# Kernel tuning notes

Hardware: AMD Instinct MI355X
Metric: run time of the kernel (lower is better)

The kernel has to match this reference:

```python
import jax, jax.numpy as jnp
import numpy as np

B, T, CIN = 32, 16384, 32
COUT, NB, NA = 32, 3, 2


def setup_inputs() -> dict:
    key = jax.random.key(0)
    k1, k2, k3, k4 = jax.random.split(key, 4)
    u = jax.random.normal(k1, (B, T, CIN), dtype=jnp.float32)
    x0 = jax.random.normal(k2, (B, NA, COUT), dtype=jnp.float32)
    # AR coeffs scaled small so the length-16384 IIR recurrence is stable
    a_coeff = jax.random.normal(k3, (NA, COUT), dtype=jnp.float32) * 0.05
    b_coeff = jax.random.normal(k4, (NB, CIN, COUT), dtype=jnp.float32)
    return {"u": u, "x0": x0, "a_coeff": a_coeff, "b_coeff": b_coeff}


def reference(u, x0, a_coeff, b_coeff):
    # u: [B, T, CIN], x0: [B, NA, COUT]
    b, t, cin = u.shape
    n_a, cout = a_coeff.shape
    n_b = b_coeff.shape[0]
    a_f = jnp.flip(a_coeff, axis=0)   # [NA, COUT]
    b_f = jnp.flip(b_coeff, axis=0)   # [NB, CIN, COUT]

    def step(carry, ut):
        ubuf, xbuf = carry                                   # [NB,B,CIN], [NA,B,COUT]
        ubuf = jnp.concatenate([ubuf[1:], ut[None]], axis=0)  # push current input
        xt = jnp.einsum('to,tbo->bo', a_f, xbuf) + jnp.einsum('tio,tbi->bo', b_f, ubuf)
        xbuf = jnp.concatenate([xbuf[1:], xt[None]], axis=0)
        return (ubuf, xbuf), xt

    u0 = jnp.zeros((n_b, b, cin), dtype=u.dtype)
    x0_t = jnp.transpose(x0, (1, 0, 2))                      # [NA, B, COUT]
    _, ys = jax.lax.scan(step, (u0, x0_t), jnp.transpose(u, (1, 0, 2)), unroll=3)
    return jnp.transpose(ys, (1, 0, 2))                      # [B, T, COUT]
```

## Files before the change

kernel.cpp:

```cpp
#include <hip/hip_runtime.h>
#include <hip/hip_bf16.h>

namespace {

typedef short bf16x8 __attribute__((ext_vector_type(8), may_alias));
typedef unsigned long long u64_ma __attribute__((may_alias));
typedef float f32x4_ma __attribute__((ext_vector_type(4), may_alias));
typedef __attribute__((ext_vector_type(16))) float f32x16;

constexpr int kB = 32, kT = 16384, kCin = 32, kCout = 32;
constexpr int kL = 128;
constexpr int kK = 32;
constexpr int kChunks = kT / kL;
constexpr int kWpB = 4;
constexpr int kRS = 80;
constexpr int kStageRows = 34;
constexpr int kStageB = kStageRows * kRS;
constexpr int kNT = 5;
constexpr int kTS = 36;
constexpr int kTBufB = 32 * kTS * 4;

__device__ __forceinline__ unsigned bfbits(float f) {
  return (unsigned)__builtin_bit_cast(unsigned short, __float2bfloat16(f));
}

__global__ __launch_bounds__(256, 4) void mimo_mfma10(
    const float* __restrict__ u,
    const float* __restrict__ x0,
    const float* __restrict__ a_coeff,
    const float* __restrict__ b_coeff,
    float* __restrict__ out)
{
  __shared__ char stage[kWpB][kStageB];
  __shared__ char tbuf[kWpB][kTBufB];

  const int tidx = (int)threadIdx.x;
  const int lane = tidx & 63;
  const int col  = lane & 31;
  const int g    = lane >> 5;
  const int widx = tidx >> 6;
  const int wid  = (int)blockIdx.x * kWpB + widx;
  const int b     = wid >> 7;
  const int chunk = wid & (kChunks - 1);
  const int t0     = chunk * kL;
  const int tstart = t0 - kK;

  char* Sw = &stage[widx][0];
  float* Tw = (float*)&tbuf[widx][0];

  bf16x8 Bf[3][2];
#pragma unroll
  for (int tau = 0; tau < 3; ++tau)
#pragma unroll
    for (int h = 0; h < 2; ++h) {
      const float* bp = b_coeff + (size_t)(2 - tau) * kCin * kCout
                        + (16 * g + 8 * h) * kCout + col;
      bf16x8 fr;
#pragma unroll
      for (int j = 0; j < 8; ++j)
        fr[j] = (short)__builtin_bit_cast(unsigned short, __float2bfloat16(bp[j * kCout]));
      Bf[tau][h] = fr;
    }

  const float a1 = a_coeff[col];
  const float a2 = a_coeff[kCout + col];
  float i1 = 0.f, i2 = 0.f;
  if (chunk == 0) {
    i1 = x0[(b * 2 + 1) * kCout + col];
    i2 = x0[(b * 2 + 0) * kCout + col];
  }
  float s1 = 0.f, s2 = 0.f;

  const float* ub = u + (size_t)b * kT * kCin;
  float* ob = out + (size_t)b * kT * kCout;

  auto gload = [&](int rowbase, int f) -> float4 {
    const int grow = rowbase + (f >> 3);
    if (grow >= 0)
      return *(const float4*)(ub + (size_t)grow * kCin + ((f & 7) << 2));
    float4 z; z.x = 0.f; z.y = 0.f; z.z = 0.f; z.w = 0.f;
    return z;
  };
  auto stash = [&](int f, float4 v) {
    const unsigned lo = bfbits(v.x) | (bfbits(v.y) << 16);
    const unsigned hi = bfbits(v.z) | (bfbits(v.w) << 16);
    const unsigned long long q = ((unsigned long long)hi << 32) | lo;
    *(u64_ma*)(Sw + (f >> 3) * kRS + (f & 7) * 8) = q;
  };

  {
    const int rowbase = tstart - 2;
    float4 p0 = gload(rowbase, lane);
    float4 p1 = gload(rowbase, lane + 64);
    float4 p2 = gload(rowbase, lane + 128);
    float4 p3 = gload(rowbase, lane + 192);
    float4 p4;
    if (lane < 16) p4 = gload(rowbase, lane + 256);
    stash(lane, p0);
    stash(lane + 64, p1);
    stash(lane + 128, p2);
    stash(lane + 192, p3);
    if (lane < 16) stash(lane + 256, p4);
  }
  asm volatile("" ::: "memory");

#pragma unroll
  for (int tile = 0; tile < kNT; ++tile) {
    const int tbase = tstart + 32 * tile;
    const bool last = (tile + 1 == kNT);
    const bool owned = (tile >= 1);

    float4 n0, n1, n2, n3, n4;
    if (!last) {
      const int rowbase = tbase + 30;
      n0 = gload(rowbase, lane);
      n1 = gload(rowbase, lane + 64);
      n2 = gload(rowbase, lane + 128);
      n3 = gload(rowbase, lane + 192);
      if (lane < 16) n4 = gload(rowbase, lane + 256);
    }

    f32x16 acc;
#pragma unroll
    for (int i = 0; i < 16; ++i) acc[i] = 0.f;
#pragma unroll
    for (int tau = 0; tau < 3; ++tau) {
      const char* rp = Sw + (col + tau) * kRS + 32 * g;
#pragma unroll
      for (int h = 0; h < 2; ++h) {
        const bf16x8 fa = *(const bf16x8*)(rp + 16 * h);
        acc = __builtin_amdgcn_mfma_f32_32x32x16_bf16(fa, Bf[tau][h], acc, 0, 0, 0);
      }
    }

    if (chunk == 0 && tile == 1) { s1 = i1; s2 = i2; }

    float x1 = s1, x2 = s2;
#pragma unroll
    for (int q = 0; q < 4; ++q) {
      const float o0 = __shfl_xor(acc[4 * q + 0], 32);
      const float o1 = __shfl_xor(acc[4 * q + 1], 32);
      const float o2 = __shfl_xor(acc[4 * q + 2], 32);
      const float o3 = __shfl_xor(acc[4 * q + 3], 32);
      const float va0 = g ? o0 : acc[4 * q + 0];
      const float va1 = g ? o1 : acc[4 * q + 1];
      const float va2 = g ? o2 : acc[4 * q + 2];
      const float va3 = g ? o3 : acc[4 * q + 3];
      const float ya0 = fmaf(a1, x1,  fmaf(a2, x2,  va0));
      const float ya1 = fmaf(a1, ya0, fmaf(a2, x1,  va1));
      const float ya2 = fmaf(a1, ya1, fmaf(a2, ya0, va2));
      const float ya3 = fmaf(a1, ya2, fmaf(a2, ya1, va3));
      const float vb0 = g ? acc[4 * q + 0] : o0;
      const float vb1 = g ? acc[4 * q + 1] : o1;
      const float vb2 = g ? acc[4 * q + 2] : o2;
      const float vb3 = g ? acc[4 * q + 3] : o3;
      const float yb0 = fmaf(a1, ya3, fmaf(a2, ya2, vb0));
      const float yb1 = fmaf(a1, yb0, fmaf(a2, ya3, vb1));
      const float yb2 = fmaf(a1, yb1, fmaf(a2, yb0, vb2));
      const float yb3 = fmaf(a1, yb2, fmaf(a2, yb1, vb3));
      x2 = yb2; x1 = yb3;
      if (owned) {
        const int rb = 8 * q + 4 * g;
        Tw[(rb + 0) * kTS + col] = g ? yb0 : ya0;
        Tw[(rb + 1) * kTS + col] = g ? yb1 : ya1;
        Tw[(rb + 2) * kTS + col] = g ? yb2 : ya2;
        Tw[(rb + 3) * kTS + col] = g ? yb3 : ya3;
      }
    }
    s1 = x1; s2 = x2;

    if (owned) {
      asm volatile("" ::: "memory");
#pragma unroll
      for (int p = 0; p < 4; ++p) {
        const f32x4_ma v = *(const f32x4_ma*)
            ((const char*)Tw + (8 * p + (lane >> 3)) * (kTS * 4) + (lane & 7) * 16);
        *(f32x4_ma*)(ob + (size_t)(tbase + 8 * p) * kCout + lane * 4) = v;
      }
      asm volatile("" ::: "memory");
    }

    if (!last) {
      asm volatile("" ::: "memory");
      stash(lane, n0);
      stash(lane + 64, n1);
      stash(lane + 128, n2);
      stash(lane + 192, n3);
      if (lane < 16) stash(lane + 256, n4);
      asm volatile("" ::: "memory");
    }
  }
}

}

extern "C" void kernel_launch(void* const* d_in, const int* in_sizes, int n_in,
                              void* d_out, int out_size, void* d_ws, size_t ws_size,
                              hipStream_t stream) {
  const float* u  = (const float*)d_in[0];
  const float* x0 = (const float*)d_in[1];
  const float* a  = (const float*)d_in[2];
  const float* bb = (const float*)d_in[3];
  float* out = (float*)d_out;

  dim3 grid(kB * kChunks / kWpB);
  dim3 block(256);
  hipLaunchKernelGGL(mimo_mfma10, grid, block, 0, stream, u, x0, a, bb, out);
}
```

Measured before the change: 29.44 us.

## Stage input tiles via global_load_lds DMA into triple-buffered swizzled LDS

Input rows no longer pass through registers with a bf16 conversion before the LDS store. Each wave now issues direct global-to-LDS 16-byte DMA loads into a three-deep fp32 staging ring, prefetching two tiles ahead. Manual vmcnt waits gate each tile, and an XOR column swizzle limits LDS bank conflicts. The bf16 conversion moves to after the LDS read, and negative-time rows are zero-filled afterwards. The larger fp32 ring roughly doubles LDS use, so launch bounds drop from 4 to 2 blocks per CU, and the hand-counted waits are fragile.

```diff
diff --git a/kernel.cpp b/kernel.cpp
--- a/kernel.cpp
+++ b/kernel.cpp
@@ -4,7 +4,6 @@
 namespace {
 
 typedef short bf16x8 __attribute__((ext_vector_type(8), may_alias));
-typedef unsigned long long u64_ma __attribute__((may_alias));
 typedef float f32x4_ma __attribute__((ext_vector_type(4), may_alias));
 typedef __attribute__((ext_vector_type(16))) float f32x16;
 
@@ -13,26 +12,37 @@
 constexpr int kK = 32;
 constexpr int kChunks = kT / kL;
 constexpr int kWpB = 4;
-constexpr int kRS = 80;
-constexpr int kStageRows = 34;
-constexpr int kStageB = kStageRows * kRS;
+constexpr int kRows = 34;
+constexpr int kStageF = kRows * kCin;
 constexpr int kNT = 5;
 constexpr int kTS = 36;
-constexpr int kTBufB = 32 * kTS * 4;
-
-__device__ __forceinline__ unsigned bfbits(float f) {
-  return (unsigned)__builtin_bit_cast(unsigned short, __float2bfloat16(f));
-}
-
-__global__ __launch_bounds__(256, 4) void mimo_mfma10(
+constexpr int kTBufF = 32 * kTS;
+
+__device__ __forceinline__ short f2bf(float f) {
+  return (short)__builtin_bit_cast(unsigned short, __float2bfloat16(f));
+}
+
+__device__ __forceinline__ void dma16(const float* g, float* l) {
+  __builtin_amdgcn_global_load_lds(
+      (__attribute__((address_space(1))) void*)(uintptr_t)g,
+      (__attribute__((address_space(3))) void*)l, 16, 0, 0);
+}
+
+#define VMWAIT(N)                                            \
+  do {                                                       \
+    asm volatile("s_waitcnt vmcnt(" #N ")" ::: "memory");    \
+    __builtin_amdgcn_sched_barrier(0);                       \
+  } while (0)
+
+__global__ __launch_bounds__(256, 2) void mimo_dma(
     const float* __restrict__ u,
     const float* __restrict__ x0,
     const float* __restrict__ a_coeff,
     const float* __restrict__ b_coeff,
     float* __restrict__ out)
 {
-  __shared__ char stage[kWpB][kStageB];
-  __shared__ char tbuf[kWpB][kTBufB];
+  __shared__ float stg[kWpB][3][kStageF];
+  __shared__ float tbf[kWpB][kTBufF];
 
   const int tidx = (int)threadIdx.x;
   const int lane = tidx & 63;
@@ -45,8 +55,7 @@
   const int t0     = chunk * kL;
   const int tstart = t0 - kK;
 
-  char* Sw = &stage[widx][0];
-  float* Tw = (float*)&tbuf[widx][0];
+  float* Tw = &tbf[widx][0];
 
   bf16x8 Bf[3][2];
 #pragma unroll
@@ -57,8 +66,7 @@
                         + (16 * g + 8 * h) * kCout + col;
       bf16x8 fr;
 #pragma unroll
-      for (int j = 0; j < 8; ++j)
-        fr[j] = (short)__builtin_bit_cast(unsigned short, __float2bfloat16(bp[j * kCout]));
+      for (int j = 0; j < 8; ++j) fr[j] = f2bf(bp[j * kCout]);
       Bf[tau][h] = fr;
     }
 
@@ -74,66 +82,75 @@
   const float* ub = u + (size_t)b * kT * kCin;
   float* ob = out + (size_t)b * kT * kCout;
 
-  auto gload = [&](int rowbase, int f) -> float4 {
-    const int grow = rowbase + (f >> 3);
-    if (grow >= 0)
-      return *(const float4*)(ub + (size_t)grow * kCin + ((f & 7) << 2));
-    float4 z; z.x = 0.f; z.y = 0.f; z.z = 0.f; z.w = 0.f;
-    return z;
+  auto dma_stage = [&](float* buf, int rowbase) {
+#pragma unroll
+    for (int k = 0; k < 4; ++k) {
+      const int p = k * 64 + lane;
+      const int row = p >> 3;
+      const int grow = rowbase + row;
+      const int src = (grow < 0 ? 0 : grow) * kCin + (((p & 7) ^ (row & 7)) << 2);
+      dma16(ub + src, buf + k * 256);
+    }
+    if (lane < 16) {
+      const int p = 256 + lane;
+      const int row = p >> 3;
+      const int grow = rowbase + row;
+      const int src = (grow < 0 ? 0 : grow) * kCin + (((p & 7) ^ (row & 7)) << 2);
+      dma16(ub + src, buf + 1024);
+    }
   };
-  auto stash = [&](int f, float4 v) {
-    const unsigned lo = bfbits(v.x) | (bfbits(v.y) << 16);
-    const unsigned hi = bfbits(v.z) | (bfbits(v.w) << 16);
-    const unsigned long long q = ((unsigned long long)hi << 32) | lo;
-    *(u64_ma*)(Sw + (f >> 3) * kRS + (f & 7) * 8) = q;
+  auto zero_fix = [&](float* buf, int rowbase) {
+    const int nch = (-rowbase) * 8;
+    for (int p = lane; p < nch; p += 64) {
+      f32x4_ma z; z[0] = 0.f; z[1] = 0.f; z[2] = 0.f; z[3] = 0.f;
+      *(f32x4_ma*)(buf + p * 4) = z;
+    }
   };
 
-  {
-    const int rowbase = tstart - 2;
-    float4 p0 = gload(rowbase, lane);
-    float4 p1 = gload(rowbase, lane + 64);
-    float4 p2 = gload(rowbase, lane + 128);
-    float4 p3 = gload(rowbase, lane + 192);
-    float4 p4;
-    if (lane < 16) p4 = gload(rowbase, lane + 256);
-    stash(lane, p0);
-    stash(lane + 64, p1);
-    stash(lane + 128, p2);
-    stash(lane + 192, p3);
-    if (lane < 16) stash(lane + 256, p4);
-  }
-  asm volatile("" ::: "memory");
+  dma_stage(&stg[widx][0][0], tstart - 2);
+  dma_stage(&stg[widx][1][0], tstart - 2 + 32);
 
 #pragma unroll
   for (int tile = 0; tile < kNT; ++tile) {
-    const int tbase = tstart + 32 * tile;
-    const bool last = (tile + 1 == kNT);
-    const bool owned = (tile >= 1);
-
-    float4 n0, n1, n2, n3, n4;
-    if (!last) {
-      const int rowbase = tbase + 30;
-      n0 = gload(rowbase, lane);
-      n1 = gload(rowbase, lane + 64);
-      n2 = gload(rowbase, lane + 128);
-      n3 = gload(rowbase, lane + 192);
-      if (lane < 16) n4 = gload(rowbase, lane + 256);
-    }
+    if (tile + 2 < kNT)
+      dma_stage(&stg[widx][(tile + 2) % 3][0], tstart - 2 + 32 * (tile + 2));
+
+    if (tile == 0)      VMWAIT(10);
+    else if (tile == 1) VMWAIT(10);
+    else if (tile == 2) VMWAIT(14);
+    else if (tile == 3) VMWAIT(13);
+    else                VMWAIT(8);
+
+    const int rowbase = tstart - 2 + 32 * tile;
+    float* Sf = &stg[widx][tile % 3][0];
+    if (chunk == 0 && rowbase < 0) zero_fix(Sf, rowbase);
 
     f32x16 acc;
 #pragma unroll
     for (int i = 0; i < 16; ++i) acc[i] = 0.f;
 #pragma unroll
     for (int tau = 0; tau < 3; ++tau) {
-      const char* rp = Sw + (col + tau) * kRS + 32 * g;
+      const int r = col + tau;
+      const float* rp = Sf + r * kCin;
+      const int rx = r & 7;
 #pragma unroll
       for (int h = 0; h < 2; ++h) {
-        const bf16x8 fa = *(const bf16x8*)(rp + 16 * h);
+        const int c0 = 4 * g + 2 * h;
+        const f32x4_ma lo = *(const f32x4_ma*)(rp + ((c0 ^ rx) << 2));
+        const f32x4_ma hi = *(const f32x4_ma*)(rp + (((c0 + 1) ^ rx) << 2));
+        bf16x8 fa;
+        fa[0] = f2bf(lo[0]); fa[1] = f2bf(lo[1]);
+        fa[2] = f2bf(lo[2]); fa[3] = f2bf(lo[3]);
+        fa[4] = f2bf(hi[0]); fa[5] = f2bf(hi[1]);
+        fa[6] = f2bf(hi[2]); fa[7] = f2bf(hi[3]);
         acc = __builtin_amdgcn_mfma_f32_32x32x16_bf16(fa, Bf[tau][h], acc, 0, 0, 0);
       }
     }
 
     if (chunk == 0 && tile == 1) { s1 = i1; s2 = i2; }
+
+    const bool owned = (tile >= 1);
+    const int tbase = tstart + 32 * tile;
 
     float x1 = s1, x2 = s2;
 #pragma unroll
@@ -179,16 +196,6 @@
       }
       asm volatile("" ::: "memory");
     }
-
-    if (!last) {
-      asm volatile("" ::: "memory");
-      stash(lane, n0);
-      stash(lane + 64, n1);
-      stash(lane + 128, n2);
-      stash(lane + 192, n3);
-      if (lane < 16) stash(lane + 256, n4);
-      asm volatile("" ::: "memory");
-    }
   }
 }
 
@@ -205,5 +212,5 @@
 
   dim3 grid(kB * kChunks / kWpB);
   dim3 block(256);
-  hipLaunchKernelGGL(mimo_mfma10, grid, block, 0, stream, u, x0, a, bb, out);
-}
+  hipLaunchKernelGGL(mimo_dma, grid, block, 0, stream, u, x0, a, bb, out);
+}
```

After: 30.07 us. 1.02x slower.

## Double-buffer LDS staging and prefetch input tiles two ahead

Applied to the files above, without the earlier changes.

Splits the per-wave LDS staging area into two buffers and keeps two register sets of prefetched input rows. Global loads are issued two tiles ahead, and the next tile is stashed into the alternate buffer, so load latency overlaps more compute. This costs more registers (another ten float4 per lane) and doubles the staging LDS, which could lower occupancy under the 4-blocks-per-CU launch bound.

```diff
diff --git a/kernel.cpp b/kernel.cpp
--- a/kernel.cpp
+++ b/kernel.cpp
@@ -18,21 +18,21 @@
 constexpr int kStageB = kStageRows * kRS;
 constexpr int kNT = 5;
 constexpr int kTS = 36;
-constexpr int kTBufB = 32 * kTS * 4;
+constexpr int kTBufF = 32 * kTS;
 
 __device__ __forceinline__ unsigned bfbits(float f) {
   return (unsigned)__builtin_bit_cast(unsigned short, __float2bfloat16(f));
 }
 
-__global__ __launch_bounds__(256, 4) void mimo_mfma10(
+__global__ __launch_bounds__(256, 4) void mimo_mfma11(
     const float* __restrict__ u,
     const float* __restrict__ x0,
     const float* __restrict__ a_coeff,
     const float* __restrict__ b_coeff,
     float* __restrict__ out)
 {
-  __shared__ char stage[kWpB][kStageB];
-  __shared__ char tbuf[kWpB][kTBufB];
+  __shared__ char stage[kWpB][2][kStageB];
+  __shared__ float tbf[kWpB][kTBufF];
 
   const int tidx = (int)threadIdx.x;
   const int lane = tidx & 63;
@@ -45,8 +45,7 @@
   const int t0     = chunk * kL;
   const int tstart = t0 - kK;
 
-  char* Sw = &stage[widx][0];
-  float* Tw = (float*)&tbuf[widx][0];
+  float* Tw = &tbf[widx][0];
 
   bf16x8 Bf[3][2];
 #pragma unroll
@@ -81,43 +80,50 @@
     float4 z; z.x = 0.f; z.y = 0.f; z.z = 0.f; z.w = 0.f;
     return z;
   };
-  auto stash = [&](int f, float4 v) {
+  auto stash = [&](char* S, int f, float4 v) {
     const unsigned lo = bfbits(v.x) | (bfbits(v.y) << 16);
     const unsigned hi = bfbits(v.z) | (bfbits(v.w) << 16);
     const unsigned long long q = ((unsigned long long)hi << 32) | lo;
-    *(u64_ma*)(Sw + (f >> 3) * kRS + (f & 7) * 8) = q;
+    *(u64_ma*)(S + (f >> 3) * kRS + (f & 7) * 8) = q;
   };
 
+  float4 pf[2][5];
+
   {
-    const int rowbase = tstart - 2;
-    float4 p0 = gload(rowbase, lane);
-    float4 p1 = gload(rowbase, lane + 64);
-    float4 p2 = gload(rowbase, lane + 128);
-    float4 p3 = gload(rowbase, lane + 192);
-    float4 p4;
-    if (lane < 16) p4 = gload(rowbase, lane + 256);
-    stash(lane, p0);
-    stash(lane + 64, p1);
-    stash(lane + 128, p2);
-    stash(lane + 192, p3);
-    if (lane < 16) stash(lane + 256, p4);
+    const int rb0 = tstart - 2;
+    pf[0][0] = gload(rb0, lane);
+    pf[0][1] = gload(rb0, lane + 64);
+    pf[0][2] = gload(rb0, lane + 128);
+    pf[0][3] = gload(rb0, lane + 192);
+    if (lane < 16) pf[0][4] = gload(rb0, lane + 256);
+    const int rb1 = tstart + 30;
+    pf[1][0] = gload(rb1, lane);
+    pf[1][1] = gload(rb1, lane + 64);
+    pf[1][2] = gload(rb1, lane + 128);
+    pf[1][3] = gload(rb1, lane + 192);
+    if (lane < 16) pf[1][4] = gload(rb1, lane + 256);
+    char* S0 = &stage[widx][0][0];
+    stash(S0, lane, pf[0][0]);
+    stash(S0, lane + 64, pf[0][1]);
+    stash(S0, lane + 128, pf[0][2]);
+    stash(S0, lane + 192, pf[0][3]);
+    if (lane < 16) stash(S0, lane + 256, pf[0][4]);
   }
   asm volatile("" ::: "memory");
 
 #pragma unroll
   for (int tile = 0; tile < kNT; ++tile) {
     const int tbase = tstart + 32 * tile;
-    const bool last = (tile + 1 == kNT);
     const bool owned = (tile >= 1);
-
-    float4 n0, n1, n2, n3, n4;
-    if (!last) {
-      const int rowbase = tbase + 30;
-      n0 = gload(rowbase, lane);
-      n1 = gload(rowbase, lane + 64);
-      n2 = gload(rowbase, lane + 128);
-      n3 = gload(rowbase, lane + 192);
-      if (lane < 16) n4 = gload(rowbase, lane + 256);
+    char* Scur = &stage[widx][tile & 1][0];
+
+    if (tile + 2 < kNT) {
+      const int rb = tstart - 2 + 32 * (tile + 2);
+      pf[tile & 1][0] = gload(rb, lane);
+      pf[tile & 1][1] = gload(rb, lane + 64);
+      pf[tile & 1][2] = gload(rb, lane + 128);
+      pf[tile & 1][3] = gload(rb, lane + 192);
+      if (lane < 16) pf[tile & 1][4] = gload(rb, lane + 256);
     }
 
     f32x16 acc;
@@ -125,7 +131,7 @@
     for (int i = 0; i < 16; ++i) acc[i] = 0.f;
 #pragma unroll
     for (int tau = 0; tau < 3; ++tau) {
-      const char* rp = Sw + (col + tau) * kRS + 32 * g;
+      const char* rp = Scur + (col + tau) * kRS + 32 * g;
 #pragma unroll
       for (int h = 0; h < 2; ++h) {
         const bf16x8 fa = *(const bf16x8*)(rp + 16 * h);
@@ -180,13 +186,13 @@
       asm volatile("" ::: "memory");
     }
 
-    if (!last) {
-      asm volatile("" ::: "memory");
-      stash(lane, n0);
-      stash(lane + 64, n1);
-      stash(lane + 128, n2);
-      stash(lane + 192, n3);
-      if (lane < 16) stash(lane + 256, n4);
+    if (tile + 1 < kNT) {
+      char* Snxt = &stage[widx][(tile + 1) & 1][0];
+      stash(Snxt, lane, pf[(tile + 1) & 1][0]);
+      stash(Snxt, lane + 64, pf[(tile + 1) & 1][1]);
+      stash(Snxt, lane + 128, pf[(tile + 1) & 1][2]);
+      stash(Snxt, lane + 192, pf[(tile + 1) & 1][3]);
+      if (lane < 16) stash(Snxt, lane + 256, pf[(tile + 1) & 1][4]);
       asm volatile("" ::: "memory");
     }
   }
@@ -205,5 +211,5 @@
 
   dim3 grid(kB * kChunks / kWpB);
   dim3 block(256);
-  hipLaunchKernelGGL(mimo_mfma10, grid, block, 0, stream, u, x0, a, bb, out);
-}
+  hipLaunchKernelGGL(mimo_mfma11, grid, block, 0, stream, u, x0, a, bb, out);
+}
```

Result: slower. 44.14 us (+49.9%).

## Stage input in 64-row double tiles to batch global loads per phase

Applied to the files above, without the earlier changes.

The per-tile staging loop (one 32-row load and stash per tile) becomes a 66-row LDS stage that holds two tiles. Loads come in bigger batches: 66 rows up front, then 64 rows prefetched while the first two tiles compute, then 32 rows while the next two compute. This cuts the number of load/stash round trips and puts more memory requests in flight per wave. In exchange, LDS per wave roughly doubles for the stage buffer and register pressure rises from holding more prefetched float4 values, which can hurt occupancy at 4 blocks per CU.

```diff
diff --git a/kernel.cpp b/kernel.cpp
--- a/kernel.cpp
+++ b/kernel.cpp
@@ -14,17 +14,16 @@
 constexpr int kChunks = kT / kL;
 constexpr int kWpB = 4;
 constexpr int kRS = 80;
-constexpr int kStageRows = 34;
-constexpr int kStageB = kStageRows * kRS;
-constexpr int kNT = 5;
+constexpr int kSRows = 66;
+constexpr int kStageB = kSRows * kRS;
 constexpr int kTS = 36;
-constexpr int kTBufB = 32 * kTS * 4;
+constexpr int kTBufF = 32 * kTS;
 
 __device__ __forceinline__ unsigned bfbits(float f) {
   return (unsigned)__builtin_bit_cast(unsigned short, __float2bfloat16(f));
 }
 
-__global__ __launch_bounds__(256, 4) void mimo_mfma10(
+__global__ __launch_bounds__(256, 4) void mimo_mfma12(
     const float* __restrict__ u,
     const float* __restrict__ x0,
     const float* __restrict__ a_coeff,
@@ -32,7 +31,7 @@
     float* __restrict__ out)
 {
   __shared__ char stage[kWpB][kStageB];
-  __shared__ char tbuf[kWpB][kTBufB];
+  __shared__ float tbf[kWpB][kTBufF];
 
   const int tidx = (int)threadIdx.x;
   const int lane = tidx & 63;
@@ -42,11 +41,10 @@
   const int wid  = (int)blockIdx.x * kWpB + widx;
   const int b     = wid >> 7;
   const int chunk = wid & (kChunks - 1);
-  const int t0     = chunk * kL;
-  const int tstart = t0 - kK;
+  const int t0    = chunk * kL;
 
   char* Sw = &stage[widx][0];
-  float* Tw = (float*)&tbuf[widx][0];
+  float* Tw = &tbf[widx][0];
 
   bf16x8 Bf[3][2];
 #pragma unroll
@@ -88,53 +86,19 @@
     *(u64_ma*)(Sw + (f >> 3) * kRS + (f & 7) * 8) = q;
   };
 
-  {
-    const int rowbase = tstart - 2;
-    float4 p0 = gload(rowbase, lane);
-    float4 p1 = gload(rowbase, lane + 64);
-    float4 p2 = gload(rowbase, lane + 128);
-    float4 p3 = gload(rowbase, lane + 192);
-    float4 p4;
-    if (lane < 16) p4 = gload(rowbase, lane + 256);
-    stash(lane, p0);
-    stash(lane + 64, p1);
-    stash(lane + 128, p2);
-    stash(lane + 192, p3);
-    if (lane < 16) stash(lane + 256, p4);
-  }
-  asm volatile("" ::: "memory");
-
-#pragma unroll
-  for (int tile = 0; tile < kNT; ++tile) {
-    const int tbase = tstart + 32 * tile;
-    const bool last = (tile + 1 == kNT);
-    const bool owned = (tile >= 1);
-
-    float4 n0, n1, n2, n3, n4;
-    if (!last) {
-      const int rowbase = tbase + 30;
-      n0 = gload(rowbase, lane);
-      n1 = gload(rowbase, lane + 64);
-      n2 = gload(rowbase, lane + 128);
-      n3 = gload(rowbase, lane + 192);
-      if (lane < 16) n4 = gload(rowbase, lane + 256);
-    }
-
+  auto do_tile = [&](int roff, int tbase, bool owned) {
     f32x16 acc;
 #pragma unroll
     for (int i = 0; i < 16; ++i) acc[i] = 0.f;
 #pragma unroll
     for (int tau = 0; tau < 3; ++tau) {
-      const char* rp = Sw + (col + tau) * kRS + 32 * g;
+      const char* rp = Sw + (roff + col + tau) * kRS + 32 * g;
 #pragma unroll
       for (int h = 0; h < 2; ++h) {
         const bf16x8 fa = *(const bf16x8*)(rp + 16 * h);
         acc = __builtin_amdgcn_mfma_f32_32x32x16_bf16(fa, Bf[tau][h], acc, 0, 0, 0);
       }
     }
-
-    if (chunk == 0 && tile == 1) { s1 = i1; s2 = i2; }
-
     float x1 = s1, x2 = s2;
 #pragma unroll
     for (int q = 0; q < 4; ++q) {
@@ -168,7 +132,6 @@
       }
     }
     s1 = x1; s2 = x2;
-
     if (owned) {
       asm volatile("" ::: "memory");
 #pragma unroll
@@ -179,17 +142,70 @@
       }
       asm volatile("" ::: "memory");
     }
-
-    if (!last) {
-      asm volatile("" ::: "memory");
-      stash(lane, n0);
-      stash(lane + 64, n1);
-      stash(lane + 128, n2);
-      stash(lane + 192, n3);
-      if (lane < 16) stash(lane + 256, n4);
-      asm volatile("" ::: "memory");
-    }
-  }
+  };
+
+  {
+    const int rb = t0 - 34;
+    float4 p0 = gload(rb, lane);
+    float4 p1 = gload(rb, lane + 64);
+    float4 p2 = gload(rb, lane + 128);
+    float4 p3 = gload(rb, lane + 192);
+    float4 p4 = gload(rb, lane + 256);
+    float4 p5 = gload(rb, lane + 320);
+    float4 p6 = gload(rb, lane + 384);
+    float4 p7 = gload(rb, lane + 448);
+    float4 p8;
+    if (lane < 16) p8 = gload(rb, lane + 512);
+    stash(lane, p0);       stash(lane + 64, p1);
+    stash(lane + 128, p2); stash(lane + 192, p3);
+    stash(lane + 256, p4); stash(lane + 320, p5);
+    stash(lane + 384, p6); stash(lane + 448, p7);
+    if (lane < 16) stash(lane + 512, p8);
+  }
+  asm volatile("" ::: "memory");
+
+  float4 n0, n1, n2, n3, n4, n5, n6, n7, n8;
+  {
+    const int rb = t0 + 30;
+    n0 = gload(rb, lane);
+    n1 = gload(rb, lane + 64);
+    n2 = gload(rb, lane + 128);
+    n3 = gload(rb, lane + 192);
+    n4 = gload(rb, lane + 256);
+    n5 = gload(rb, lane + 320);
+    n6 = gload(rb, lane + 384);
+    n7 = gload(rb, lane + 448);
+    if (lane < 16) n8 = gload(rb, lane + 512);
+  }
+  do_tile(0, t0 - 32, false);
+  if (chunk == 0) { s1 = i1; s2 = i2; }
+  do_tile(32, t0, true);
+  asm volatile("" ::: "memory");
+  stash(lane, n0);       stash(lane + 64, n1);
+  stash(lane + 128, n2); stash(lane + 192, n3);
+  stash(lane + 256, n4); stash(lane + 320, n5);
+  stash(lane + 384, n6); stash(lane + 448, n7);
+  if (lane < 16) stash(lane + 512, n8);
+  asm volatile("" ::: "memory");
+
+  float4 m0, m1, m2, m3, m4;
+  {
+    const int rb = t0 + 94;
+    m0 = gload(rb, lane);
+    m1 = gload(rb, lane + 64);
+    m2 = gload(rb, lane + 128);
+    m3 = gload(rb, lane + 192);
+    if (lane < 16) m4 = gload(rb, lane + 256);
+  }
+  do_tile(0, t0 + 32, true);
+  do_tile(32, t0 + 64, true);
+  asm volatile("" ::: "memory");
+  stash(lane, m0);       stash(lane + 64, m1);
+  stash(lane + 128, m2); stash(lane + 192, m3);
+  if (lane < 16) stash(lane + 256, m4);
+  asm volatile("" ::: "memory");
+
+  do_tile(0, t0 + 96, true);
 }
 
 }
@@ -205,5 +221,5 @@
 
   dim3 grid(kB * kChunks / kWpB);
   dim3 block(256);
-  hipLaunchKernelGGL(mimo_mfma10, grid, block, 0, stream, u, x0, a, bb, out);
-}
+  hipLaunchKernelGGL(mimo_mfma12, grid, block, 0, stream, u, x0, a, bb, out);
+}
```

Measured after the change: 42.08 us. 1.43x slower.
